# Performance work log

Hardware: AMD Instinct MI355X
Metric: run time of the kernel (lower is better)

## Reference

```python
import jax, jax.numpy as jnp
import numpy as np

NEG_SLOPE = 0.2


def _segment_softmax(logits, seg, num_segments):
    m = jax.ops.segment_max(logits, seg, num_segments=num_segments)
    m = jnp.where(jnp.isfinite(m), m, 0.0)
    e = jnp.exp(logits - m[seg])
    s = jax.ops.segment_sum(e, seg, num_segments=num_segments)
    return e / (s[seg] + 1e-16)


def _gat_conv(x, src, dst, W, a_src, a_dst, b, num_nodes):
    # PyG GATConv, heads=1, concat=True, add_self_loops already applied to src/dst.
    h = x @ W                                  # [N, F_out]
    alpha_src = h @ a_src                      # [N]
    alpha_dst = h @ a_dst                      # [N]
    logits = jax.nn.leaky_relu(alpha_src[src] + alpha_dst[dst], NEG_SLOPE)  # [E]
    alpha = _segment_softmax(logits, dst, num_nodes)                        # [E]
    out = jax.ops.segment_sum(alpha[:, None] * h[src], dst, num_segments=num_nodes)
    return out + b


def setup_inputs() -> dict:
    key = jax.random.key(0)
    ks = jax.random.split(key, 16)
    N, E, F_in = 50000, 1600000, 256
    x = jax.random.normal(ks[0], (N, F_in), dtype=jnp.float32)
    edge_index = jax.random.randint(ks[1], (2, E), 0, N, dtype=jnp.int64)
    edge_attr = jax.random.normal(ks[2], (E, 1), dtype=jnp.float32)

    def glorot(k, shape):
        fan = sum(shape) if len(shape) > 1 else shape[0]
        return jax.random.normal(k, shape, dtype=jnp.float32) * jnp.sqrt(2.0 / fan)

    params = {
        "W1": glorot(ks[3], (F_in, 48)), "as1": glorot(ks[4], (48,)),
        "ad1": glorot(ks[5], (48,)),     "b1": jnp.zeros((48,), jnp.float32),
        "W2": glorot(ks[6], (48, 60)),   "as2": glorot(ks[7], (60,)),
        "ad2": glorot(ks[8], (60,)),     "b2": jnp.zeros((60,), jnp.float32),
        "W3": glorot(ks[9], (60, 1)),    "as3": glorot(ks[10], (1,)),
        "ad3": glorot(ks[11], (1,)),     "b3": jnp.zeros((1,), jnp.float32),
    }
    return {"x": x, "edge_index": edge_index, "edge_attr": edge_attr, **params}


def reference(x, edge_index, edge_attr, W1, as1, ad1, b1, W2, as2, ad2, b2, W3, as3, ad3, b3):
    # edge_attr is accepted but ignored: GATConv was built without edge_dim, so no lin_edge.
    N = x.shape[0]
    loops = jnp.arange(N, dtype=edge_index.dtype)
    src = jnp.concatenate([edge_index[0], loops])  # add_self_loops=True
    dst = jnp.concatenate([edge_index[1], loops])
    h = jax.nn.relu(_gat_conv(x, src, dst, W1, as1, ad1, b1, N))
    h = jax.nn.relu(_gat_conv(h, src, dst, W2, as2, ad2, b2, N))
    h = _gat_conv(h, src, dst, W3, as3, ad3, b3, N)
    return h.reshape(-1)  # flatten -> [N]
```

## Files before the change

kernel.cpp:

```cpp
#include <hip/hip_runtime.h>
#include <cstdint>
#include <cstddef>


__device__ __forceinline__ float leaky(float v) { return v > 0.f ? v : 0.2f * v; }

__device__ __forceinline__ unsigned short f2bf(float x) {
    unsigned int u = __float_as_uint(x);
    u = (u + 0x7FFFu + ((u >> 16) & 1u)) >> 16;
    return (unsigned short)u;
}
__device__ __forceinline__ float bf2f(unsigned short b) {
    return __uint_as_float(((unsigned int)b) << 16);
}
__device__ __forceinline__ float bfhi(unsigned int d) {
    return __uint_as_float(d & 0xFFFF0000u);
}
__device__ __forceinline__ float bflo(unsigned int d) {
    return __uint_as_float(d << 16);
}

typedef _Float16 half8 __attribute__((ext_vector_type(8)));
typedef float f32x4 __attribute__((ext_vector_type(4)));

#define BSHIFT 7
#define BCAP   5120
#define CTILE  8192


__global__ __launch_bounds__(256) void coarse_bin_kernel(
    const int* __restrict__ ei, unsigned int* __restrict__ staged,
    int* __restrict__ gcursor, int E, int K) {
    __shared__ int hist[512];
    __shared__ int rank[512];
    __shared__ int base[512];
    for (int b = threadIdx.x; b < K; b += 256) { hist[b] = 0; rank[b] = 0; }
    __syncthreads();

    int e0 = blockIdx.x * CTILE;
    int e1 = min(E, e0 + CTILE);

    for (int e = e0 + threadIdx.x; e < e1; e += 256) {
        int d = ei[E + e];
        atomicAdd(&hist[d >> BSHIFT], 1);
    }
    __syncthreads();

    for (int b = threadIdx.x; b < K; b += 256) {
        int c = hist[b];
        base[b] = c ? atomicAdd(&gcursor[b], c) : 0;
    }
    __syncthreads();

    for (int e = e0 + threadIdx.x; e < e1; e += 256) {
        int s = ei[e];
        int d = ei[E + e];
        int b = d >> BSHIFT;
        int r = atomicAdd(&rank[b], 1);
        staged[(size_t)b * BCAP + base[b] + r] =
            ((unsigned int)(d & ((1 << BSHIFT) - 1)) << 16) | (unsigned int)s;
    }
}


__global__ __launch_bounds__(512) void bucket_scan_kernel(
    const int* __restrict__ gcursor, int* __restrict__ bbase, int K) {
    __shared__ int sh[512];
    int t = threadIdx.x;
    int v = (t < K) ? gcursor[t] : 0;
    sh[t] = v;
    __syncthreads();
    for (int off = 1; off < 512; off <<= 1) {
        int a = (t >= off) ? sh[t - off] : 0;
        __syncthreads();
        sh[t] += a;
        __syncthreads();
    }
    if (t < K) bbase[t] = sh[t] - v;
}


__global__ __launch_bounds__(256) void fine_sort_kernel(
    const unsigned int* __restrict__ staged, const int* __restrict__ gcursor,
    const int* __restrict__ bbase, int* __restrict__ rowptr, int* __restrict__ csr,
    int N, int E) {
    __shared__ int cnt[128];
    __shared__ int off[128];
    __shared__ int lcsr[BCAP];
    const int b = blockIdx.x;
    const int t = threadIdx.x;
    const int c = gcursor[b];
    const int gb = bbase[b];
    const unsigned int* rec = staged + (size_t)b * BCAP;

    if (t < 128) cnt[t] = 0;
    __syncthreads();

    for (int i = t; i < c; i += 256) atomicAdd(&cnt[rec[i] >> 16], 1);
    __syncthreads();

    if (t < 128) off[t] = cnt[t];
    __syncthreads();
    for (int s = 1; s < 128; s <<= 1) {
        int a = (t >= s && t < 128) ? off[t - s] : 0;
        __syncthreads();
        if (t < 128) off[t] += a;
        __syncthreads();
    }

    if (t < 128) {
        int excl = off[t] - cnt[t];
        int n = (b << BSHIFT) + t;
        if (n <= N) rowptr[n] = gb + excl;
        cnt[t] = excl;
    }
    if (b == 0 && t == 0) rowptr[N] = E;
    __syncthreads();

    for (int i = t; i < c; i += 256) {
        unsigned int r = rec[i];
        int p = atomicAdd(&cnt[r >> 16], 1);
        lcsr[p] = (int)(r & 0xFFFFu);
    }
    __syncthreads();

    for (int i = t; i < c; i += 256) csr[gb + i] = lcsr[i];
}


template <int FIN>
__global__ __launch_bounds__(256) void gemm1_mfma_kernel(
    const float* __restrict__ X, const float* __restrict__ W,
    const float* __restrict__ avs, const float* __restrict__ avd,
    unsigned short* __restrict__ hb, float* __restrict__ asrc, float* __restrict__ adst,
    int N) {
    constexpr int FOUT = 48;
    constexpr int KK = FIN / 32;
    static_assert(FIN % 32 == 0, "FIN multiple of 32");

    const int wid  = __builtin_amdgcn_readfirstlane(threadIdx.x >> 6);
    const int lane = threadIdx.x & 63;
    const int col  = lane & 15;
    const int grp  = lane >> 4;
    const int wbase = blockIdx.x * 64 + wid * 16;

    int arow = wbase + col;
    if (arow >= N) arow = N - 1;
    const float* xrow = X + (size_t)arow * FIN + grp * 8;

    half8 Bf[3][KK];
#pragma unroll
    for (int t = 0; t < 3; t++) {
#pragma unroll
        for (int kk = 0; kk < KK; kk++) {
            const float* wp = W + (size_t)(kk * 32 + grp * 8) * FOUT + t * 16 + col;
#pragma unroll
            for (int j = 0; j < 8; j++)
                Bf[t][kk][j] = (_Float16)wp[(size_t)j * FOUT];
        }
    }

    f32x4 acc0 = {0.f, 0.f, 0.f, 0.f};
    f32x4 acc1 = {0.f, 0.f, 0.f, 0.f};
    f32x4 acc2 = {0.f, 0.f, 0.f, 0.f};

#pragma unroll
    for (int kk = 0; kk < KK; kk++) {
        float4 xa = *(const float4*)(xrow + kk * 32);
        float4 xb = *(const float4*)(xrow + kk * 32 + 4);
        float xs[8] = {xa.x, xa.y, xa.z, xa.w, xb.x, xb.y, xb.z, xb.w};
        half8 ah, al;
#pragma unroll
        for (int j = 0; j < 8; j++) {
            _Float16 h = (_Float16)xs[j];
            ah[j] = h;
            al[j] = (_Float16)(xs[j] - (float)h);
        }
        acc0 = __builtin_amdgcn_mfma_f32_16x16x32_f16(ah, Bf[0][kk], acc0, 0, 0, 0);
        acc1 = __builtin_amdgcn_mfma_f32_16x16x32_f16(ah, Bf[1][kk], acc1, 0, 0, 0);
        acc2 = __builtin_amdgcn_mfma_f32_16x16x32_f16(ah, Bf[2][kk], acc2, 0, 0, 0);
        acc0 = __builtin_amdgcn_mfma_f32_16x16x32_f16(al, Bf[0][kk], acc0, 0, 0, 0);
        acc1 = __builtin_amdgcn_mfma_f32_16x16x32_f16(al, Bf[1][kk], acc1, 0, 0, 0);
        acc2 = __builtin_amdgcn_mfma_f32_16x16x32_f16(al, Bf[2][kk], acc2, 0, 0, 0);
    }

    float avs0 = avs[col], avs1 = avs[16 + col], avs2 = avs[32 + col];
    float avd0 = avd[col], avd1 = avd[16 + col], avd2 = avd[32 + col];

#pragma unroll
    for (int r = 0; r < 4; r++) {
        float ps = acc0[r] * avs0 + acc1[r] * avs1 + acc2[r] * avs2;
        float pd = acc0[r] * avd0 + acc1[r] * avd1 + acc2[r] * avd2;
#pragma unroll
        for (int off = 8; off; off >>= 1) {
            ps += __shfl_xor(ps, off, 64);
            pd += __shfl_xor(pd, off, 64);
        }
        int nd = wbase + grp * 4 + r;
        if (col == r && nd < N) { asrc[nd] = ps; adst[nd] = pd; }
    }

#pragma unroll
    for (int r = 0; r < 4; r++) {
        int nd = wbase + grp * 4 + r;
        if (nd < N) {
            unsigned short* hp = hb + (size_t)nd * 64 + col;
            hp[0]  = f2bf(acc0[r]);
            hp[16] = f2bf(acc1[r]);
            hp[32] = f2bf(acc2[r]);
        }
    }
}


template <int FIN, int FOUT, int FT>
__global__ __launch_bounds__(256) void gemm_sgpr_kernel(
    const float* __restrict__ X, const float* __restrict__ W,
    const float* __restrict__ avs, const float* __restrict__ avd,
    unsigned short* __restrict__ hb, float* __restrict__ asrc, float* __restrict__ adst,
    int N) {
    static_assert(4 * FT == FOUT, "FT must be FOUT/4");
    __shared__ float red[2][4][64];

    const int wid  = __builtin_amdgcn_readfirstlane(threadIdx.x >> 6);
    const int lane = threadIdx.x & 63;
    const int n    = blockIdx.x * 64 + lane;
    const int nc   = (n < N) ? n : N - 1;
    const int fbase = wid * FT;

    const float* xrow = X + (size_t)nc * FIN;

    float acc[FT];
#pragma unroll
    for (int c = 0; c < FT; c++) acc[c] = 0.f;

#pragma unroll
    for (int k = 0; k < FIN; k += 4) {
        float4 xv = *(const float4*)(xrow + k);
        const float* w0 = W + (size_t)k * FOUT + fbase;
#pragma unroll
        for (int c = 0; c < FT; c++) {
            acc[c] = fmaf(xv.x, w0[c],            acc[c]);
            acc[c] = fmaf(xv.y, w0[FOUT + c],     acc[c]);
            acc[c] = fmaf(xv.z, w0[2 * FOUT + c], acc[c]);
            acc[c] = fmaf(xv.w, w0[3 * FOUT + c], acc[c]);
        }
    }

    float ps = 0.f, pd = 0.f;
#pragma unroll
    for (int c = 0; c < FT; c++) {
        ps = fmaf(acc[c], avs[fbase + c], ps);
        pd = fmaf(acc[c], avd[fbase + c], pd);
    }
    red[0][wid][lane] = ps;
    red[1][wid][lane] = pd;

    if (n < N) {
        if constexpr ((FT & 1) == 0) {
            unsigned int* dst = (unsigned int*)(hb + (size_t)n * 64 + fbase);
#pragma unroll
            for (int c = 0; c < FT; c += 2) {
                unsigned int pk = (unsigned int)f2bf(acc[c]) |
                                  ((unsigned int)f2bf(acc[c + 1]) << 16);
                dst[c >> 1] = pk;
            }
        } else {
#pragma unroll
            for (int c = 0; c < FT; c++)
                hb[(size_t)n * 64 + fbase + c] = f2bf(acc[c]);
        }
    }

    __syncthreads();
    if (threadIdx.x < 64 && n < N) {
        float s = red[0][0][lane] + red[0][1][lane] + red[0][2][lane] + red[0][3][lane];
        float d = red[1][0][lane] + red[1][1][lane] + red[1][2][lane] + red[1][3][lane];
        asrc[n] = s;
        adst[n] = d;
    }
}


#define CHUNK 128

template <int FOUT, bool RELU>
__global__ __launch_bounds__(256) void agg_quad_kernel(
    const int* __restrict__ rowptr, const int* __restrict__ csr,
    const float* __restrict__ asrc, const float* __restrict__ adst,
    const unsigned short* __restrict__ hb, const float* __restrict__ bias,
    float* __restrict__ OUT, int N) {
    constexpr int NSUB = FOUT / 4;
    static_assert(FOUT % 4 == 0, "FOUT multiple of 4");
    __shared__ int2 wslds[4][CHUNK];
    const int wv = threadIdx.x >> 6;
    int n = blockIdx.x * 4 + wv;
    if (n >= N) return;
    const int lane = threadIdx.x & 63;
    const int q    = lane >> 4;
    const int sub  = lane & 15;
    const unsigned int suboff = (unsigned int)sub * 8;
    const int rs = rowptr[n], re = rowptr[n + 1];
    const float ad_n = adst[n];
    const float wself = __expf(leaky(asrc[n] + ad_n));
    const char* hbb = (const char*)hb;

    float a0 = 0.f, a1 = 0.f, a2 = 0.f, a3 = 0.f;
    float wpart = 0.f;

    for (int base = rs; base < re; base += CHUNK) {
        const int cnt = min(CHUNK, re - base);
        if (lane < cnt) {
            int s = csr[base + lane];
            float w = __expf(leaky(asrc[s] + ad_n));
            wpart += w;
            wslds[wv][lane] = make_int2(s << 7, __float_as_int(w));
        }
        int i = 0;
        for (; i + 4 <= cnt; i += 4) {
            int2 p = wslds[wv][i + q];
            uint2 dv = *(const uint2*)(hbb + ((unsigned int)p.x + suboff));
            float w = __int_as_float(p.y);
            a0 = fmaf(w, bflo(dv.x), a0);
            a1 = fmaf(w, bfhi(dv.x), a1);
            a2 = fmaf(w, bflo(dv.y), a2);
            a3 = fmaf(w, bfhi(dv.y), a3);
        }
        const int rem = cnt - i;
        if (rem) {
            int2 p = wslds[wv][i + ((q < rem) ? q : 0)];
            uint2 dv = *(const uint2*)(hbb + ((unsigned int)p.x + suboff));
            float w = (q < rem) ? __int_as_float(p.y) : 0.f;
            a0 = fmaf(w, bflo(dv.x), a0);
            a1 = fmaf(w, bfhi(dv.x), a1);
            a2 = fmaf(w, bflo(dv.y), a2);
            a3 = fmaf(w, bfhi(dv.y), a3);
        }
    }

#pragma unroll
    for (int off = 32; off; off >>= 1) wpart += __shfl_xor(wpart, off, 64);
    const float ssum = wpart + wself;

    a0 += __shfl_xor(a0, 16, 64); a0 += __shfl_xor(a0, 32, 64);
    a1 += __shfl_xor(a1, 16, 64); a1 += __shfl_xor(a1, 32, 64);
    a2 += __shfl_xor(a2, 16, 64); a2 += __shfl_xor(a2, 32, 64);
    a3 += __shfl_xor(a3, 16, 64); a3 += __shfl_xor(a3, 32, 64);

    {
        uint2 sv = *(const uint2*)(hbb + (((unsigned int)n << 7) + suboff));
        a0 = fmaf(wself, bflo(sv.x), a0);
        a1 = fmaf(wself, bfhi(sv.x), a1);
        a2 = fmaf(wself, bflo(sv.y), a2);
        a3 = fmaf(wself, bfhi(sv.y), a3);
    }

    if (lane < NSUB) {
        const float inv = 1.f / (ssum + 1e-16f);
        float4 bv = *(const float4*)(bias + sub * 4);
        float4 o;
        o.x = a0 * inv + bv.x;
        o.y = a1 * inv + bv.y;
        o.z = a2 * inv + bv.z;
        o.w = a3 * inv + bv.w;
        if (RELU) {
            o.x = fmaxf(o.x, 0.f); o.y = fmaxf(o.y, 0.f);
            o.z = fmaxf(o.z, 0.f); o.w = fmaxf(o.w, 0.f);
        }
        *(float4*)(OUT + (size_t)n * FOUT + sub * 4) = o;
    }
}


__global__ __launch_bounds__(256) void agg_quad_h3_kernel(
    const int* __restrict__ rowptr, const int* __restrict__ csr,
    const float* __restrict__ asrc, const float* __restrict__ adst,
    const unsigned short* __restrict__ hb, const float* __restrict__ bias,
    const float* __restrict__ W3, float* __restrict__ h3, int N) {
    constexpr int FOUT = 60;
    constexpr int NSUB = FOUT / 4;
    __shared__ int2 wslds[4][CHUNK];
    const int wv = threadIdx.x >> 6;
    int n = blockIdx.x * 4 + wv;
    if (n >= N) return;
    const int lane = threadIdx.x & 63;
    const int q    = lane >> 4;
    const int sub  = lane & 15;
    const unsigned int suboff = (unsigned int)sub * 8;
    const int rs = rowptr[n], re = rowptr[n + 1];
    const float ad_n = adst[n];
    const float wself = __expf(leaky(asrc[n] + ad_n));
    const char* hbb = (const char*)hb;

    float a0 = 0.f, a1 = 0.f, a2 = 0.f, a3 = 0.f;
    float wpart = 0.f;

    for (int base = rs; base < re; base += CHUNK) {
        const int cnt = min(CHUNK, re - base);
        if (lane < cnt) {
            int s = csr[base + lane];
            float w = __expf(leaky(asrc[s] + ad_n));
            wpart += w;
            wslds[wv][lane] = make_int2(s << 7, __float_as_int(w));
        }
        int i = 0;
        for (; i + 4 <= cnt; i += 4) {
            int2 p = wslds[wv][i + q];
            uint2 dv = *(const uint2*)(hbb + ((unsigned int)p.x + suboff));
            float w = __int_as_float(p.y);
            a0 = fmaf(w, bflo(dv.x), a0);
            a1 = fmaf(w, bfhi(dv.x), a1);
            a2 = fmaf(w, bflo(dv.y), a2);
            a3 = fmaf(w, bfhi(dv.y), a3);
        }
        const int rem = cnt - i;
        if (rem) {
            int2 p = wslds[wv][i + ((q < rem) ? q : 0)];
            uint2 dv = *(const uint2*)(hbb + ((unsigned int)p.x + suboff));
            float w = (q < rem) ? __int_as_float(p.y) : 0.f;
            a0 = fmaf(w, bflo(dv.x), a0);
            a1 = fmaf(w, bfhi(dv.x), a1);
            a2 = fmaf(w, bflo(dv.y), a2);
            a3 = fmaf(w, bfhi(dv.y), a3);
        }
    }

#pragma unroll
    for (int off = 32; off; off >>= 1) wpart += __shfl_xor(wpart, off, 64);
    const float ssum = wpart + wself;

    a0 += __shfl_xor(a0, 16, 64); a0 += __shfl_xor(a0, 32, 64);
    a1 += __shfl_xor(a1, 16, 64); a1 += __shfl_xor(a1, 32, 64);
    a2 += __shfl_xor(a2, 16, 64); a2 += __shfl_xor(a2, 32, 64);
    a3 += __shfl_xor(a3, 16, 64); a3 += __shfl_xor(a3, 32, 64);

    {
        uint2 sv = *(const uint2*)(hbb + (((unsigned int)n << 7) + suboff));
        a0 = fmaf(wself, bflo(sv.x), a0);
        a1 = fmaf(wself, bfhi(sv.x), a1);
        a2 = fmaf(wself, bflo(sv.y), a2);
        a3 = fmaf(wself, bfhi(sv.y), a3);
    }

    float t = 0.f;
    {
        const int subc = (sub < NSUB) ? sub : 0;
        const float inv = 1.f / (ssum + 1e-16f);
        float4 bv = *(const float4*)(bias + subc * 4);
        float4 wv3 = *(const float4*)(W3 + subc * 4);
        float o0 = fmaxf(a0 * inv + bv.x, 0.f);
        float o1 = fmaxf(a1 * inv + bv.y, 0.f);
        float o2 = fmaxf(a2 * inv + bv.z, 0.f);
        float o3 = fmaxf(a3 * inv + bv.w, 0.f);
        if (sub < NSUB)
            t = o0 * wv3.x + o1 * wv3.y + o2 * wv3.z + o3 * wv3.w;
    }
#pragma unroll
    for (int off = 8; off; off >>= 1) t += __shfl_xor(t, off, 64);
    if (lane == 0) h3[n] = t;
}


__global__ __launch_bounds__(256) void agg1_kernel(
    const int* __restrict__ rowptr, const int* __restrict__ csr,
    const float* __restrict__ h3,
    const float* __restrict__ as3p, const float* __restrict__ ad3p,
    const float* __restrict__ bias, float* __restrict__ OUT, int N) {
    int n = blockIdx.x * 4 + (threadIdx.x >> 6);
    if (n >= N) return;
    int lane = threadIdx.x & 63;
    int rs = rowptr[n], re = rowptr[n + 1];
    const float a_s = as3p[0];
    float hn = h3[n];
    float adn = ad3p[0] * hn;
    float wself = __expf(leaky(a_s * hn + adn));

    float ssum = 0.f, accv = 0.f;
    for (int e = rs + lane; e < re; e += 64) {
        float hs = h3[csr[e]];
        float w = __expf(leaky(a_s * hs + adn));
        ssum += w;
        accv = fmaf(w, hs, accv);
    }
#pragma unroll
    for (int off = 32; off; off >>= 1) {
        ssum += __shfl_xor(ssum, off, 64);
        accv += __shfl_xor(accv, off, 64);
    }
    ssum += wself;
    accv = fmaf(wself, hn, accv);
    if (lane == 0) OUT[n] = accv / (ssum + 1e-16f) + bias[0];
}


extern "C" void kernel_launch(void* const* d_in, const int* in_sizes, int n_in,
                              void* d_out, int out_size, void* d_ws, size_t ws_size,
                              hipStream_t stream) {
    const float* x      = (const float*)d_in[0];
    const int*   ei     = (const int*)d_in[1];
    const float* W1  = (const float*)d_in[3];
    const float* as1 = (const float*)d_in[4];
    const float* ad1 = (const float*)d_in[5];
    const float* b1  = (const float*)d_in[6];
    const float* W2  = (const float*)d_in[7];
    const float* as2 = (const float*)d_in[8];
    const float* ad2 = (const float*)d_in[9];
    const float* b2  = (const float*)d_in[10];
    const float* W3  = (const float*)d_in[11];
    const float* as3 = (const float*)d_in[12];
    const float* ad3 = (const float*)d_in[13];
    const float* b3  = (const float*)d_in[14];

    const int N = in_sizes[0] / 256;
    const int E = in_sizes[1] / 2;
    const int K = (N + (1 << BSHIFT) - 1) >> BSHIFT;

    char* p = (char*)d_ws;
    auto alloc = [&](size_t bytes) -> void* {
        void* r = (void*)p;
        p += ((bytes + 255) / 256) * 256;
        return r;
    };
    int*   gcursor = (int*)alloc(512 * 4);
    int*   bbase   = (int*)alloc(512 * 4);
    int*   rowptr  = (int*)alloc(((size_t)N + 1) * 4);
    int*   csr     = (int*)alloc((size_t)E * 4);
    unsigned short* hb = (unsigned short*)alloc((size_t)N * 64 * 2);
    float* actbuf  = (float*)alloc((size_t)N * 48 * 4);
    float* h3      = (float*)alloc((size_t)N * 4);
    float* asrc    = (float*)alloc((size_t)N * 4);
    float* adst    = (float*)alloc((size_t)N * 4);
    unsigned int* staged = (unsigned int*)actbuf;

    hipMemsetAsync(gcursor, 0, 512 * 4, stream);
    int cblocks = (E + CTILE - 1) / CTILE;
    coarse_bin_kernel<<<cblocks, 256, 0, stream>>>(ei, staged, gcursor, E, K);
    bucket_scan_kernel<<<1, 512, 0, stream>>>(gcursor, bbase, K);
    fine_sort_kernel<<<K, 256, 0, stream>>>(staged, gcursor, bbase, rowptr, csr, N, E);

    int gblocks = (N + 63) / 64;
    int ablocks = (N + 3) / 4;

    gemm1_mfma_kernel<256><<<gblocks, 256, 0, stream>>>(
        x, W1, as1, ad1, hb, asrc, adst, N);
    agg_quad_kernel<48, true><<<ablocks, 256, 0, stream>>>(rowptr, csr, asrc, adst, hb, b1, actbuf, N);

    gemm_sgpr_kernel<48, 60, 15><<<gblocks, 256, 0, stream>>>(
        actbuf, W2, as2, ad2, hb, asrc, adst, N);
    agg_quad_h3_kernel<<<ablocks, 256, 0, stream>>>(rowptr, csr, asrc, adst, hb, b2, W3, h3, N);

    agg1_kernel<<<ablocks, 256, 0, stream>>>(rowptr, csr, h3, as3, ad3, b3, (float*)d_out, N);
}
```

Measured before the change: 283.6 us.

## Software-pipeline edge gathers in aggregation kernels with batched unrolled loads

Reworks the two GAT aggregation kernels so each wave processes up to 64 edges per chunk. It first writes the source offsets to LDS, then issues 8 or 16 independent feature gathers before computing the exp attention weights, which overlaps the exp math with gather latency. Padding lanes point at the node itself with zero weight, so there are no remainder branches. Out-of-range feature subgroups are clamped to valid columns. The cost is extra work on padded edges when a node's degree is small, and higher register pressure from the unrolled gathers.

```diff
diff --git a/kernel.cpp b/kernel.cpp
--- a/kernel.cpp
+++ b/kernel.cpp
@@ -282,24 +282,48 @@
 }
 
 
-#define CHUNK 128
+#define GATHER_STEP(NG)                                                        \
+    {                                                                          \
+        int   off_[NG];                                                        \
+        uint2 hd_[NG];                                                         \
+        float ww_[NG];                                                         \
+        _Pragma("unroll")                                                      \
+        for (int u = 0; u < NG; u++) off_[u] = offlds[wv][4 * u + q];          \
+        _Pragma("unroll")                                                      \
+        for (int u = 0; u < NG; u++)                                           \
+            hd_[u] = *(const uint2*)(hbb + ((unsigned int)off_[u] + suboff));  \
+        float we = (lane < cnt) ? __expf(leaky(as + ad_n)) : 0.f;              \
+        wpart += we;                                                           \
+        wlds[wv][lane] = we;                                                   \
+        _Pragma("unroll")                                                      \
+        for (int u = 0; u < NG; u++) ww_[u] = wlds[wv][4 * u + q];             \
+        _Pragma("unroll")                                                      \
+        for (int u = 0; u < NG; u++) {                                         \
+            a0 = fmaf(ww_[u], bflo(hd_[u].x), a0);                             \
+            a1 = fmaf(ww_[u], bfhi(hd_[u].x), a1);                             \
+            a2 = fmaf(ww_[u], bflo(hd_[u].y), a2);                             \
+            a3 = fmaf(ww_[u], bfhi(hd_[u].y), a3);                             \
+        }                                                                      \
+    }
 
 template <int FOUT, bool RELU>
-__global__ __launch_bounds__(256) void agg_quad_kernel(
+__global__ __launch_bounds__(256) void agg_pipe_kernel(
     const int* __restrict__ rowptr, const int* __restrict__ csr,
     const float* __restrict__ asrc, const float* __restrict__ adst,
     const unsigned short* __restrict__ hb, const float* __restrict__ bias,
     float* __restrict__ OUT, int N) {
     constexpr int NSUB = FOUT / 4;
     static_assert(FOUT % 4 == 0, "FOUT multiple of 4");
-    __shared__ int2 wslds[4][CHUNK];
+    __shared__ int   offlds[4][64];
+    __shared__ float wlds[4][64];
     const int wv = threadIdx.x >> 6;
     int n = blockIdx.x * 4 + wv;
     if (n >= N) return;
     const int lane = threadIdx.x & 63;
     const int q    = lane >> 4;
     const int sub  = lane & 15;
-    const unsigned int suboff = (unsigned int)sub * 8;
+    const int subc = (sub < NSUB) ? sub : NSUB - 1;
+    const unsigned int suboff = (unsigned int)subc * 8;
     const int rs = rowptr[n], re = rowptr[n + 1];
     const float ad_n = adst[n];
     const float wself = __expf(leaky(asrc[n] + ad_n));
@@ -308,34 +332,15 @@
     float a0 = 0.f, a1 = 0.f, a2 = 0.f, a3 = 0.f;
     float wpart = 0.f;
 
-    for (int base = rs; base < re; base += CHUNK) {
-        const int cnt = min(CHUNK, re - base);
-        if (lane < cnt) {
-            int s = csr[base + lane];
-            float w = __expf(leaky(asrc[s] + ad_n));
-            wpart += w;
-            wslds[wv][lane] = make_int2(s << 7, __float_as_int(w));
-        }
-        int i = 0;
-        for (; i + 4 <= cnt; i += 4) {
-            int2 p = wslds[wv][i + q];
-            uint2 dv = *(const uint2*)(hbb + ((unsigned int)p.x + suboff));
-            float w = __int_as_float(p.y);
-            a0 = fmaf(w, bflo(dv.x), a0);
-            a1 = fmaf(w, bfhi(dv.x), a1);
-            a2 = fmaf(w, bflo(dv.y), a2);
-            a3 = fmaf(w, bfhi(dv.y), a3);
-        }
-        const int rem = cnt - i;
-        if (rem) {
-            int2 p = wslds[wv][i + ((q < rem) ? q : 0)];
-            uint2 dv = *(const uint2*)(hbb + ((unsigned int)p.x + suboff));
-            float w = (q < rem) ? __int_as_float(p.y) : 0.f;
-            a0 = fmaf(w, bflo(dv.x), a0);
-            a1 = fmaf(w, bfhi(dv.x), a1);
-            a2 = fmaf(w, bflo(dv.y), a2);
-            a3 = fmaf(w, bfhi(dv.y), a3);
-        }
+    for (int base = rs; base < re; base += 64) {
+        const int cnt = min(64, re - base);
+        int ce = base + lane;
+        if (ce >= re) ce = re - 1;
+        int sv = csr[ce];
+        int sidx = (lane < cnt) ? sv : n;
+        offlds[wv][lane] = sidx << 7;
+        float as = asrc[sidx];
+        if (cnt <= 32) { GATHER_STEP(8) } else { GATHER_STEP(16) }
     }
 
 #pragma unroll
@@ -372,21 +377,23 @@
 }
 
 
-__global__ __launch_bounds__(256) void agg_quad_h3_kernel(
+__global__ __launch_bounds__(256) void agg_pipe_h3_kernel(
     const int* __restrict__ rowptr, const int* __restrict__ csr,
     const float* __restrict__ asrc, const float* __restrict__ adst,
     const unsigned short* __restrict__ hb, const float* __restrict__ bias,
     const float* __restrict__ W3, float* __restrict__ h3, int N) {
     constexpr int FOUT = 60;
     constexpr int NSUB = FOUT / 4;
-    __shared__ int2 wslds[4][CHUNK];
+    __shared__ int   offlds[4][64];
+    __shared__ float wlds[4][64];
     const int wv = threadIdx.x >> 6;
     int n = blockIdx.x * 4 + wv;
     if (n >= N) return;
     const int lane = threadIdx.x & 63;
     const int q    = lane >> 4;
     const int sub  = lane & 15;
-    const unsigned int suboff = (unsigned int)sub * 8;
+    const int subc = (sub < NSUB) ? sub : NSUB - 1;
+    const unsigned int suboff = (unsigned int)subc * 8;
     const int rs = rowptr[n], re = rowptr[n + 1];
     const float ad_n = adst[n];
     const float wself = __expf(leaky(asrc[n] + ad_n));
@@ -395,34 +402,15 @@
     float a0 = 0.f, a1 = 0.f, a2 = 0.f, a3 = 0.f;
     float wpart = 0.f;
 
-    for (int base = rs; base < re; base += CHUNK) {
-        const int cnt = min(CHUNK, re - base);
-        if (lane < cnt) {
-            int s = csr[base + lane];
-            float w = __expf(leaky(asrc[s] + ad_n));
-            wpart += w;
-            wslds[wv][lane] = make_int2(s << 7, __float_as_int(w));
-        }
-        int i = 0;
-        for (; i + 4 <= cnt; i += 4) {
-            int2 p = wslds[wv][i + q];
-            uint2 dv = *(const uint2*)(hbb + ((unsigned int)p.x + suboff));
-            float w = __int_as_float(p.y);
-            a0 = fmaf(w, bflo(dv.x), a0);
-            a1 = fmaf(w, bfhi(dv.x), a1);
-            a2 = fmaf(w, bflo(dv.y), a2);
-            a3 = fmaf(w, bfhi(dv.y), a3);
-        }
-        const int rem = cnt - i;
-        if (rem) {
-            int2 p = wslds[wv][i + ((q < rem) ? q : 0)];
-            uint2 dv = *(const uint2*)(hbb + ((unsigned int)p.x + suboff));
-            float w = (q < rem) ? __int_as_float(p.y) : 0.f;
-            a0 = fmaf(w, bflo(dv.x), a0);
-            a1 = fmaf(w, bfhi(dv.x), a1);
-            a2 = fmaf(w, bflo(dv.y), a2);
-            a3 = fmaf(w, bfhi(dv.y), a3);
-        }
+    for (int base = rs; base < re; base += 64) {
+        const int cnt = min(64, re - base);
+        int ce = base + lane;
+        if (ce >= re) ce = re - 1;
+        int sv = csr[ce];
+        int sidx = (lane < cnt) ? sv : n;
+        offlds[wv][lane] = sidx << 7;
+        float as = asrc[sidx];
+        if (cnt <= 32) { GATHER_STEP(8) } else { GATHER_STEP(16) }
     }
 
 #pragma unroll
@@ -444,7 +432,6 @@
 
     float t = 0.f;
     {
-        const int subc = (sub < NSUB) ? sub : 0;
         const float inv = 1.f / (ssum + 1e-16f);
         float4 bv = *(const float4*)(bias + subc * 4);
         float4 wv3 = *(const float4*)(W3 + subc * 4);
@@ -543,11 +530,11 @@
 
     gemm1_mfma_kernel<256><<<gblocks, 256, 0, stream>>>(
         x, W1, as1, ad1, hb, asrc, adst, N);
-    agg_quad_kernel<48, true><<<ablocks, 256, 0, stream>>>(rowptr, csr, asrc, adst, hb, b1, actbuf, N);
+    agg_pipe_kernel<48, true><<<ablocks, 256, 0, stream>>>(rowptr, csr, asrc, adst, hb, b1, actbuf, N);
 
     gemm_sgpr_kernel<48, 60, 15><<<gblocks, 256, 0, stream>>>(
         actbuf, W2, as2, ad2, hb, asrc, adst, N);
-    agg_quad_h3_kernel<<<ablocks, 256, 0, stream>>>(rowptr, csr, asrc, adst, hb, b2, W3, h3, N);
+    agg_pipe_h3_kernel<<<ablocks, 256, 0, stream>>>(rowptr, csr, asrc, adst, hb, b2, W3, h3, N);
 
     agg1_kernel<<<ablocks, 256, 0, stream>>>(rowptr, csr, h3, as3, ad3, b3, (float*)d_out, N);
 }
```

Result: faster. 267.6 us (-5.6%).
